# Kernel tuning notes

Hardware: AMD Instinct MI355X
Metric: run time of the kernel (lower is better)

Reference implementation:

```python
import math
import jax, jax.numpy as jnp
import numpy as np

GRAIN = 300   # bilinear / grain dim (gpconv output channels)
PAD = 4       # explicit zero padding before each conv1d / conv2d
POOL = 40     # adaptive pool target (mf_model_pool_dim)

def conv1d_k2(x, w, b):
    # x: [B, L, Cin], w: [Cout, Cin, 2] -> [B, L-1, Cout]
    return (jnp.einsum('blc,oc->blo', x[:, :-1], w[:, :, 0])
            + jnp.einsum('blc,oc->blo', x[:, 1:], w[:, :, 1]) + b)

def kmax_last(x, k):
    # torch-style k-max pooling: top-k values along last axis, original order kept
    idx = jnp.sort(jax.lax.top_k(x, k)[1], axis=-1)
    return jnp.take_along_axis(x, idx, axis=-1)

def kmax_len(x, k):
    # k-max pooling over the length axis (axis=1) of [B, L, C]
    return jnp.swapaxes(kmax_last(jnp.swapaxes(x, 1, 2), k), 1, 2)

def adaptive_max_1d(x, out, axis):
    # torch AdaptiveMaxPool semantics along one axis; windows precomputed statically
    L = x.shape[axis]
    r = np.arange(out)
    starts = (r * L) // out
    ends = -((-(r + 1) * L) // out)
    maxw = int((ends - starts).max())
    off = starts[:, None] + np.arange(maxw)[None, :]
    mask = jnp.asarray(off < ends[:, None])
    idxs = np.minimum(off, L - 1)
    xm = jnp.moveaxis(x, axis, -1)
    g = jnp.where(mask, xm[..., idxs], -jnp.inf)
    return jnp.moveaxis(g.max(-1), -1, axis)

def conv2d_p4(x, w, b):
    y = jax.lax.conv_general_dilated(x, w, (1, 1), [(PAD, PAD), (PAD, PAD)],
                                     dimension_numbers=('NCHW', 'OIHW', 'NCHW'))
    return y + b[None, :, None, None]

def gp_tower(x, w1, b1, w2, b2, w3, b3, k1, k2):
    # multigranular conv tower: zero-pad(4) -> conv1d(k=2) -> tanh -> k-max pool
    g0 = kmax_last(x, GRAIN)                      # [B, L, 300]
    def block(z, w, b, k):
        z = jnp.pad(z, ((0, 0), (PAD, PAD), (0, 0)))
        return kmax_len(jnp.tanh(conv1d_k2(z, w, b)), k)
    p1 = block(x, w1, b1, k1)                     # [B, k1, 300]
    p2 = block(p1, w2, b2, k2)                    # [B, k2, 300]
    p3 = block(p2, w3, b3, 1)                     # [B, 1, 300]
    return jnp.concatenate([g0, p1, p2, p3], axis=1)

def _forward(query, pos_doc, neg_docs, qw1, qb1, qw2, qb2, qw3, qb3,
             dw1, db1, dw2, db2, dw3, db3, bw, bb,
             mw1, mb1, mw2, mb2, mw3, mb3, lw, lb):
    B, Lq, _ = query.shape
    S, _, Ld, _ = neg_docs.shape
    kq1, kq2 = max(4, math.ceil(2 * Lq / 3)), max(4, math.ceil(Lq / 3))
    kd1, kd2 = max(4, math.ceil(2 * Ld / 3)), max(4, math.ceil(Ld / 3))
    qg = gp_tower(query, qw1, qb1, qw2, qb2, qw3, qb3, kq1, kq2)   # [B, Nq, 300]
    docs = jnp.concatenate([pos_doc[None], neg_docs], 0).reshape((S + 1) * B, Ld, -1)
    dg = gp_tower(docs, dw1, db1, dw2, db2, dw3, db3, kd1, kd2)    # [(S+1)B, Nd, 300]
    Nq, Nd = qg.shape[1], dg.shape[1]
    dg = dg.reshape(S + 1, B, Nd, GRAIN)
    # batched bilinear matching + sigmoid (replaces the O(Nq*Nd) per-pair loop)
    qt = jnp.einsum('bqd,de->bqe', qg, bw)
    M = jax.nn.sigmoid(jnp.einsum('bqe,sbje->sbqj', qt, dg) + bb[0])
    M = M.reshape((S + 1) * B, Nq, Nd)
    x = adaptive_max_1d(adaptive_max_1d(M, POOL, 1), POOL, 2)[:, None]  # [N,1,40,40]
    for w, b in ((mw1, mb1), (mw2, mb2), (mw3, mb3)):
        x = jax.nn.sigmoid(conv2d_p4(x, w, b))
        x = adaptive_max_1d(adaptive_max_1d(x, POOL, 2), POOL, 3)
        x = x.max(axis=1, keepdims=True)          # k-max(k=1) over channels
    feat = x[:, 0]                                # [N, 40, 40]
    h = jax.nn.sigmoid(jnp.einsum('nij,j->ni', feat, lw[0]) + lb[0])
    s = jax.nn.sigmoid(h @ lw[0] + lb[0])
    return s.reshape(S + 1, B)                    # row 0 = pos-doc scores

def setup_inputs():
    ks = jax.random.split(jax.random.key(0), 26)
    def n(i, shape, s=0.05):
        return jax.random.normal(ks[i], shape, dtype=jnp.float32) * s
    return dict(
        query=jax.random.normal(ks[0], (16, 239, 1024), dtype=jnp.float32),
        pos_doc=jax.random.normal(ks[1], (16, 479, 1024), dtype=jnp.float32),
        neg_docs=jax.random.normal(ks[2], (4, 16, 479, 1024), dtype=jnp.float32),
        qw1=n(3, (300, 1024, 2)), qb1=n(4, (300,)),
        qw2=n(5, (300, 300, 2)), qb2=n(6, (300,)),
        qw3=n(7, (300, 300, 2)), qb3=n(8, (300,)),
        dw1=n(9, (300, 1024, 2)), db1=n(10, (300,)),
        dw2=n(11, (300, 300, 2)), db2=n(12, (300,)),
        dw3=n(13, (300, 300, 2)), db3=n(14, (300,)),
        bw=n(15, (300, 300)), bb=n(16, (1,)),
        mw1=n(17, (50, 1, 2, 2)), mb1=n(18, (50,)),
        mw2=n(19, (50, 1, 2, 2)), mb2=n(20, (50,)),
        mw3=n(21, (50, 1, 2, 2)), mb3=n(22, (50,)),
        lw=n(23, (1, 40)), lb=n(24, (1,)),
    )

def reference(query, pos_doc, neg_docs, qw1, qb1, qw2, qb2, qw3, qb3,
              dw1, db1, dw2, db2, dw3, db3, bw, bb,
              mw1, mb1, mw2, mb2, mw3, mb3, lw, lb):
    return _forward(query, pos_doc, neg_docs, qw1, qb1, qw2, qb2, qw3, qb3,
                    dw1, db1, dw2, db2, dw3, db3, bw, bb,
                    mw1, mb1, mw2, mb2, mw3, mb3, lw, lb)
```

## Files before the change

kernel.cpp:

```cpp
#include <hip/hip_runtime.h>
#include <hip/hip_bf16.h>
#include <math.h>

typedef unsigned long long ull;
typedef unsigned int uint;
typedef unsigned short ushort_t;

typedef short bf16x8 __attribute__((ext_vector_type(8)));
typedef float floatx4 __attribute__((ext_vector_type(4)));

__device__ inline ushort_t f2b(float f) {
    uint u = __float_as_uint(f);
    u = u + 0x7fffu + ((u >> 16) & 1u);
    return (ushort_t)(u >> 16);
}

__device__ inline uint kmap16(ushort_t u) {
    return (u & 0x8000u) ? (uint)((~u) & 0xFFFFu) : (uint)(u | 0x8000u);
}
__device__ inline ushort_t kinv16(uint k) {
    return (k & 0x8000u) ? (ushort_t)(k ^ 0x8000u) : (ushort_t)((~k) & 0xFFFFu);
}

__device__ inline void async_copy16(const void* g, void* l) {
    __builtin_amdgcn_global_load_lds(
        (const __attribute__((address_space(1))) void*)g,
        (__attribute__((address_space(3))) void*)l, 16, 0, 0);
}

__global__ void prep_w2_kernel(const float* __restrict__ w, ushort_t* __restrict__ Wb,
                               int C, int CP) {
    int CHn = CP / 32;
    int total = CHn * 2 * 20 * 512;
    for (int i = blockIdx.x * blockDim.x + threadIdx.x; i < total;
         i += gridDim.x * blockDim.x) {
        int e = i & 7;
        int lane = (i >> 3) & 63;
        int rest = i >> 9;
        int g = rest % 20;
        int tc = rest / 20;
        int t = tc & 1, c = tc >> 1;
        int o = g * 16 + (lane & 15);
        int ch = c * 32 + (lane >> 4) * 8 + e;
        float v = (o < 300 && ch < C) ? w[((size_t)o * C + ch) * 2 + t] : 0.f;
        Wb[i] = f2b(v);
    }
}

__global__ void prep_bw_kernel(const float* __restrict__ bw, ushort_t* __restrict__ bwb) {
    int i = blockIdx.x * 256 + threadIdx.x;
    if (i >= 320 * 320) return;
    int e = i / 320, d = i - e * 320;
    bwb[i] = (e < 300 && d < 300) ? f2b(bw[d * 300 + e]) : (ushort_t)0;
}

__global__ __launch_bounds__(256) void x_pad_bf16_kernel(
    const float* __restrict__ src, const float* __restrict__ src2, int split_n,
    long long s_nstr, int Lin, ushort_t* __restrict__ dst, int rows)
{
    int r = blockIdx.x, n = blockIdx.y;
    const float* sp = (split_n > 0 && n >= split_n)
                          ? src2 + (size_t)(n - split_n) * s_nstr
                          : src + (size_t)n * s_nstr;
    int g = r - 4;
    ushort_t* dp = dst + ((size_t)n * rows + r) * 1024;
    int c = threadIdx.x * 4;
    ushort4 o = {0, 0, 0, 0};
    if (g >= 0 && g < Lin) {
        float4 v = *(const float4*)&sp[(size_t)g * 1024 + c];
        o.x = f2b(v.x); o.y = f2b(v.y); o.z = f2b(v.z); o.w = f2b(v.w);
    }
    *(ushort4*)&dp[c] = o;
}

template <int CP>
__global__ __launch_bounds__(256, 2) void conv_lds_kernel(
    const ushort_t* __restrict__ xq, long long xq_nstr,
    const ushort_t* __restrict__ xd, long long xd_nstr,
    const ushort_t* __restrict__ Wq, const ushort_t* __restrict__ Wd,
    const float* __restrict__ bq, const float* __restrict__ bd,
    int Lout_q, int Lout_d, int mtiles_q,
    ushort_t* __restrict__ yt)
{
    constexpr int CH = CP / 32;
    constexpr int BUFB = 65 * 64;
    __shared__ ushort_t Abuf[3][65 * 32];

    int mt = blockIdx.x, n = blockIdx.y;
    bool isq = (n < 16);
    if (isq && mt >= mtiles_q) return;
    const ushort_t* x = isq ? xq + (size_t)n * xq_nstr
                            : xd + (size_t)(n - 16) * xd_nstr;
    const ushort_t* W = isq ? Wq : Wd;
    const float* bias = isq ? bq : bd;
    int Lout = isq ? Lout_q : Lout_d;
    int l0 = mt * 64;

    int tid = threadIdx.x, wid = tid >> 6, lane = tid & 63;
    int wn = wid * 80;
    int lrow = lane & 15, quad = lane >> 4;

    int srow = tid >> 2;
    int sslot = (tid & 3) ^ ((tid >> 3) & 3);
    const ushort_t* gMain = x + (size_t)(l0 + srow) * CP + sslot * 8;
    const ushort_t* gXtra = x + (size_t)(l0 + 64) * CP + wid * 8;

    const ushort_t* Bw = W + ((size_t)wid * 5) * 512 + lane * 8;

    int offA[2][4];
#pragma unroll
    for (int t = 0; t < 2; t++)
#pragma unroll
        for (int ms = 0; ms < 4; ms++) {
            int r = ms * 16 + lrow + t;
            offA[t][ms] = r * 64 + ((quad ^ ((r >> 1) & 3)) << 4);
        }

    floatx4 acc[4][5];
#pragma unroll
    for (int i = 0; i < 4; i++)
#pragma unroll
        for (int j = 0; j < 5; j++) acc[i][j] = (floatx4){0.f, 0.f, 0.f, 0.f};

    char* lds0 = (char*)&Abuf[0][0];

    auto STAGE = [&](int cc, int slot) {
        char* lb = lds0 + slot * BUFB;
        async_copy16(gMain + cc * 32, lb + wid * 1024);
        if (lane == 0) async_copy16(gXtra + cc * 32, lb + 4096 + wid * 16);
    };
    auto LOADB = [&](bf16x8 (&bf)[2][5], int cc) {
#pragma unroll
        for (int t = 0; t < 2; t++)
#pragma unroll
            for (int ns = 0; ns < 5; ns++)
                bf[t][ns] = *(const bf16x8*)(Bw + (size_t)((cc * 2 + t) * 20 + ns) * 512);
    };
    auto COMPUTE = [&](bf16x8 (&bf)[2][5], int rslot) {
        const char* ab = lds0 + rslot * BUFB;
        __builtin_amdgcn_s_setprio(1);
#pragma unroll
        for (int t = 0; t < 2; t++) {
            bf16x8 af[4];
#pragma unroll
            for (int ms = 0; ms < 4; ms++)
                af[ms] = *(const bf16x8*)(ab + offA[t][ms]);
#pragma unroll
            for (int ms = 0; ms < 4; ms++)
#pragma unroll
                for (int ns = 0; ns < 5; ns++)
                    acc[ms][ns] = __builtin_amdgcn_mfma_f32_16x16x32_bf16(
                        af[ms], bf[t][ns], acc[ms][ns], 0, 0, 0);
        }
        __builtin_amdgcn_s_setprio(0);
    };
    auto WAITBAR = [&]() {
        asm volatile("s_waitcnt vmcnt(10)" ::: "memory");
        __builtin_amdgcn_s_barrier();
        __builtin_amdgcn_sched_barrier(0);
    };

    bf16x8 bA[2][5], bB[2][5];

    STAGE(0, 0);
    LOADB(bA, 0);
    STAGE(1, 1);

    int sl = 0;
    for (int c = 0; c < CH; c += 2) {
        int rA = sl;
        int rB = rA + 1; if (rB == 3) rB = 0;
        int wA = rB + 1; if (wA == 3) wA = 0;
        int wB = rA;

        WAITBAR();
        LOADB(bB, c + 1);
        __builtin_amdgcn_sched_barrier(0x38F);
        if (c + 2 < CH) STAGE(c + 2, wA);
        COMPUTE(bA, rA);

        WAITBAR();
        if (c + 2 < CH) LOADB(bA, c + 2);
        __builtin_amdgcn_sched_barrier(0x38F);
        if (c + 3 < CH) STAGE(c + 3, wB);
        COMPUTE(bB, rB);

        sl = wA;
    }

    ushort_t* yp = yt + (size_t)n * (320 * 488);
#pragma unroll
    for (int ns = 0; ns < 5; ns++) {
        int o = wn + ns * 16 + lrow;
        if (o >= 300) continue;
        float bo = bias[o];
        ushort_t* orow = yp + (size_t)o * 488;
#pragma unroll
        for (int ms = 0; ms < 4; ms++) {
            int l = l0 + ms * 16 + quad * 4;
            if (l + 3 < Lout) {
                ushort4 v;
                v.x = f2b(tanhf(acc[ms][ns][0] + bo));
                v.y = f2b(tanhf(acc[ms][ns][1] + bo));
                v.z = f2b(tanhf(acc[ms][ns][2] + bo));
                v.w = f2b(tanhf(acc[ms][ns][3] + bo));
                *(ushort4*)&orow[l] = v;
            } else {
#pragma unroll
                for (int r = 0; r < 4; r++)
                    if (l + r < Lout) orow[l + r] = f2b(tanhf(acc[ms][ns][r] + bo));
            }
        }
    }
}

template <int EPT>
__global__ __launch_bounds__(256) void topk16_kernel(
    const ushort_t* __restrict__ src, int CC,
    long long s_n, long long s_c, long long s_e,
    int L, int k,
    ushort_t* __restrict__ out1, long long o1_off, long long o1_n,
    long long o1_c, long long o1_e,
    ushort_t* __restrict__ out2, long long o2_off, long long o2_n,
    long long o2_c, long long o2_e)
{
    __shared__ uint sbuf[257];
    __shared__ uint wtot[4];
    __shared__ uint bsel[2];
    __shared__ uint wsum[4];

    int row = blockIdx.x;
    int n = row / CC, c = row - n * CC;
    const ushort_t* sp = src + (size_t)n * s_n + (size_t)c * s_c;

    int tid = threadIdx.x, lane = tid & 63, wid = tid >> 6;
    int base = tid * EPT;

    uint key[EPT];
    if (EPT == 4 && s_e == 1) {
        ushort4 v = *(const ushort4*)&sp[base];
        key[0] = kmap16(v.x); key[1] = kmap16(v.y);
        key[2] = kmap16(v.z); key[3] = kmap16(v.w);
    } else {
#pragma unroll
        for (int e = 0; e < EPT; e++) {
            int i = base + e;
            key[e] = (i < L) ? kmap16(sp[(size_t)i * s_e]) : 0u;
        }
    }

    uint pmask = 0, pval = 0, rem = (uint)k;
#pragma unroll
    for (int shift = 8; shift >= 0; shift -= 8) {
        sbuf[tid] = 0;
        __syncthreads();
#pragma unroll
        for (int e = 0; e < EPT; e++) {
            int i = base + e;
            if (i < L && (key[e] & pmask) == pval)
                atomicAdd(&sbuf[(key[e] >> shift) & 255], 1u);
        }
        __syncthreads();
        uint sfx = sbuf[tid];
#pragma unroll
        for (int off = 1; off < 64; off <<= 1) {
            uint u2 = __shfl_down(sfx, off);
            if (lane + off < 64) sfx += u2;
        }
        if (lane == 0) wtot[wid] = sfx;
        __syncthreads();
        uint hi = 0;
        for (int w = wid + 1; w < 4; w++) hi += wtot[w];
        sbuf[tid] = sfx + hi;
        if (tid == 0) sbuf[256] = 0;
        __syncthreads();
        uint cg = sbuf[tid], cgn = sbuf[tid + 1];
        if (cg >= rem && cgn < rem) { bsel[0] = (uint)tid; bsel[1] = rem - cgn; }
        __syncthreads();
        pval |= bsel[0] << shift;
        pmask |= 0xFFu << shift;
        rem = bsel[1];
        __syncthreads();
    }

    const uint T = pval;
    uint gtc = 0, eqc = 0;
#pragma unroll
    for (int e = 0; e < EPT; e++) {
        int i = base + e;
        if (i < L) {
            gtc += (key[e] > T) ? 1u : 0u;
            eqc += (key[e] == T) ? 1u : 0u;
        }
    }
    uint pack = (gtc << 16) | eqc;
    uint incl = pack;
#pragma unroll
    for (int off = 1; off < 64; off <<= 1) {
        uint u2 = __shfl_up(incl, off);
        if (lane >= off) incl += u2;
    }
    uint excl = incl - pack;
    if (lane == 63) wsum[wid] = incl;
    __syncthreads();
    uint badd = 0;
    for (int w = 0; w < wid; w++) badd += wsum[w];
    excl += badd;
    uint gt_before = excl >> 16, eq_before = excl & 0xffffu;

    ushort_t* dp1 = out1 + (size_t)o1_off + (size_t)n * o1_n + (size_t)c * o1_c;
    ushort_t* dp2 = out2 ? out2 + (size_t)o2_off + (size_t)n * o2_n + (size_t)c * o2_c
                         : (ushort_t*)0;
#pragma unroll
    for (int e = 0; e < EPT; e++) {
        int i = base + e;
        if (i >= L) break;
        uint kk = key[e];
        if (kk > T) {
            uint pos = gt_before + (eq_before < rem ? eq_before : rem);
            ushort_t v = kinv16(kk);
            dp1[(size_t)pos * o1_e] = v;
            if (dp2) dp2[(size_t)pos * o2_e] = v;
            gt_before++;
        } else if (kk == T) {
            if (eq_before < rem) {
                uint pos = gt_before + eq_before;
                ushort_t v = kinv16(kk);
                dp1[(size_t)pos * o1_e] = v;
                if (dp2) dp2[(size_t)pos * o2_e] = v;
            }
            eq_before++;
        }
    }
}

__global__ __launch_bounds__(256) void topk_cols_kernel(
    const ushort_t* __restrict__ yt2,
    int Lq, int Ld, int kq, int kd,
    ushort_t* __restrict__ qg, int qoff,
    ushort_t* __restrict__ dg, int doff,
    ushort_t* __restrict__ pq, long long pq_nstr,
    ushort_t* __restrict__ pd, long long pd_nstr)
{
    __shared__ __align__(16) ushort_t xin[32][488];
    __shared__ __align__(16) uint hist[32 * 257];
    ushort_t* otile = (ushort_t*)hist;

    int cg = blockIdx.x, n = blockIdx.y;
    int c0 = cg * 32;
    bool isq = (n < 16);
    int L = isq ? Lq : Ld;
    int k = isq ? kq : kd;
    int nd = isq ? n : n - 16;
    int tid = threadIdx.x;

    const ushort_t* src = yt2 + (size_t)n * (320 * 488) + (size_t)c0 * 488;
    for (int i = tid; i < 32 * 61; i += 256) {
        int j = i / 61, s = i - j * 61;
        *(uint4*)&xin[j][s * 8] = *(const uint4*)&src[(size_t)j * 488 + s * 8];
    }
    __syncthreads();

    int g = tid >> 3, r = tid & 7;
    uint* hg = &hist[g * 257];
    bool cval = (c0 + g) < 300;
    int S = (L + 7) >> 3;
    int llo = r * S, lhi = llo + S;
    if (lhi > L) lhi = L;
    if (llo > L) llo = L;

    uint rem = (uint)k;
    uint bsel = 0;
    uint Tt = 0;

#pragma unroll
    for (int round = 0; round < 2; round++) {
        for (int t = r; t < 256; t += 8) hg[t] = 0;
        for (int l = llo; l < lhi; l++) {
            uint key = cval ? kmap16(xin[g][l]) : 0x8000u;
            if (round == 0)
                atomicAdd(&hg[key >> 8], 1u);
            else if ((key >> 8) == bsel)
                atomicAdd(&hg[key & 255u], 1u);
        }
        uint hv[32];
        uint Sr = 0;
        int b0 = r * 32;
#pragma unroll
        for (int t = 0; t < 32; t++) { hv[t] = hg[b0 + t]; Sr += hv[t]; }
        uint suf = Sr;
#pragma unroll
        for (int off = 1; off < 8; off <<= 1) {
            uint u = __shfl_down(suf, off);
            if (r + off < 8) suf += u;
        }
        uint acc = suf - Sr;
        uint found = 0;
#pragma unroll
        for (int t = 31; t >= 0; t--) {
            uint h = hv[t];
            if (!found && acc < rem && acc + h >= rem)
                found = ((uint)(b0 + t) << 16) | (rem - acc);
            acc += h;
        }
#pragma unroll
        for (int off = 1; off < 8; off <<= 1) found |= __shfl_xor(found, off);
        if (round == 0) {
            bsel = found >> 16;
            rem = found & 0xffffu;
        } else {
            Tt = (bsel << 8) | (found >> 16);
            rem = found & 0xffffu;
        }
    }

    uint gtc = 0, eqc = 0;
    for (int l = llo; l < lhi; l++) {
        uint key = cval ? kmap16(xin[g][l]) : 0x8000u;
        gtc += (key > Tt) ? 1u : 0u;
        eqc += (key == Tt) ? 1u : 0u;
    }
    uint pack = (gtc << 16) | eqc, incl = pack;
#pragma unroll
    for (int off = 1; off < 8; off <<= 1) {
        uint u = __shfl_up(incl, off);
        if (r >= off) incl += u;
    }
    uint excl = incl - pack;
    uint gt_b = excl >> 16, eq_b = excl & 0xffffu;

    __syncthreads();

    for (int l = llo; l < lhi; l++) {
        uint key = cval ? kmap16(xin[g][l]) : 0x8000u;
        if (key > Tt) {
            uint pos = gt_b + (eq_b < rem ? eq_b : rem);
            otile[pos * 32 + g] = kinv16(key);
            gt_b++;
        } else if (key == Tt) {
            if (eq_b < rem) otile[(gt_b + eq_b) * 32 + g] = kinv16(key);
            eq_b++;
        }
    }
    __syncthreads();

    ushort_t* d1 = isq ? qg + ((size_t)nd * 480 + qoff) * 320 + c0
                       : dg + ((size_t)nd * 960 + doff) * 320 + c0;
    ushort_t* d2 = 0;
    if (isq) { if (pq) d2 = pq + (size_t)nd * pq_nstr + 4 * 320 + c0; }
    else     { if (pd) d2 = pd + (size_t)nd * pd_nstr + 4 * 320 + c0; }

    for (int i = tid; i < k * 8; i += 256) {
        int p = i >> 3, s = i & 7;
        ushort4 v = *(ushort4*)&otile[p * 32 + s * 4];
        *(ushort4*)&d1[(size_t)p * 320 + s * 4] = v;
        if (d2) *(ushort4*)&d2[(size_t)p * 320 + s * 4] = v;
    }
}

__global__ __launch_bounds__(256) void qt_mfma_kernel(
    const ushort_t* __restrict__ qgb, const ushort_t* __restrict__ bwb,
    ushort_t* __restrict__ qtb)
{
    int mt = blockIdx.x, b = blockIdx.y;
    int tid = threadIdx.x, wid = tid >> 6, lane = tid & 63;
    int wn = wid * 80, lrow = lane & 15, quad = lane >> 4;

    const ushort_t* A = qgb + ((size_t)b * 480 + mt * 48 + lrow) * 320 + quad * 8;
    const ushort_t* B = bwb + (size_t)(wn + lrow) * 320 + quad * 8;

    floatx4 acc[3][5];
#pragma unroll
    for (int i = 0; i < 3; i++)
#pragma unroll
        for (int j = 0; j < 5; j++) acc[i][j] = (floatx4){0.f, 0.f, 0.f, 0.f};

#pragma unroll 5
    for (int c0 = 0; c0 < 320; c0 += 32) {
        bf16x8 af[3], bfr[5];
#pragma unroll
        for (int ms = 0; ms < 3; ms++)
            af[ms] = *(const bf16x8*)&A[(size_t)(ms * 16) * 320 + c0];
#pragma unroll
        for (int ns = 0; ns < 5; ns++)
            bfr[ns] = *(const bf16x8*)&B[(size_t)(ns * 16) * 320 + c0];
#pragma unroll
        for (int ms = 0; ms < 3; ms++)
#pragma unroll
            for (int ns = 0; ns < 5; ns++)
                acc[ms][ns] = __builtin_amdgcn_mfma_f32_16x16x32_bf16(
                    af[ms], bfr[ns], acc[ms][ns], 0, 0, 0);
    }

    ushort_t* out = qtb + ((size_t)b * 480 + mt * 48) * 320;
#pragma unroll
    for (int ms = 0; ms < 3; ms++)
#pragma unroll
        for (int ns = 0; ns < 5; ns++)
#pragma unroll
            for (int r = 0; r < 4; r++)
                out[(size_t)(ms * 16 + quad * 4 + r) * 320 + wn + ns * 16 + lrow] =
                    f2b(acc[ms][ns][r]);
}

__global__ __launch_bounds__(256) void mpool_mfma_kernel(
    const ushort_t* __restrict__ qtb16, const ushort_t* __restrict__ dgb16,
    const float* __restrict__ bb, float* __restrict__ mp)
{
    __shared__ float pool[2 * 12 * 192];

    int jb = blockIdx.x;
    int qb = blockIdx.y;
    int n  = blockIdx.z;
    int b  = n & 15;

    int tid = threadIdx.x;
    int wid = tid >> 6, lane = tid & 63;
    int wm2 = wid >> 1;
    int wm = wm2 * 48, wn = (wid & 1) * 96;
    int lrow = lane & 15, quad = lane >> 4;

    const ushort_t* Abase = qtb16 + ((size_t)b * 480 + qb * 96 + wm) * 320 + quad * 8;
    const ushort_t* Bbase = dgb16 + ((size_t)n * 960 + jb * 192 + wn) * 320 + quad * 8;

    floatx4 acc[3][6];
#pragma unroll
    for (int i = 0; i < 3; i++)
#pragma unroll
        for (int j = 0; j < 6; j++) acc[i][j] = (floatx4){0.f, 0.f, 0.f, 0.f};

#pragma unroll 2
    for (int c0 = 0; c0 < 320; c0 += 32) {
        bf16x8 af[3], bfr[6];
#pragma unroll
        for (int mt = 0; mt < 3; mt++)
            af[mt] = *(const bf16x8*)&Abase[(size_t)(mt * 16 + lrow) * 320 + c0];
#pragma unroll
        for (int nt = 0; nt < 6; nt++)
            bfr[nt] = *(const bf16x8*)&Bbase[(size_t)(nt * 16 + lrow) * 320 + c0];
#pragma unroll
        for (int mt = 0; mt < 3; mt++)
#pragma unroll
            for (int nt = 0; nt < 6; nt++)
                acc[mt][nt] = __builtin_amdgcn_mfma_f32_16x16x32_bf16(
                    af[mt], bfr[nt], acc[mt][nt], 0, 0, 0);
    }

#pragma unroll
    for (int mt = 0; mt < 3; mt++) {
        int g = mt * 4 + quad;
#pragma unroll
        for (int nt = 0; nt < 6; nt++) {
            floatx4 a = acc[mt][nt];
            float rm = fmaxf(fmaxf(a[0], a[1]), fmaxf(a[2], a[3]));
            pool[(wm2 * 12 + g) * 192 + wn + nt * 16 + lrow] = rm;
        }
    }
    __syncthreads();

    if (tid < 64) {
        int qw = tid >> 3, jw = tid & 7;
        int slab = qw >> 2, w = qw & 3;
        float m = -INFINITY;
        const float* pp = &pool[(slab * 12 + w * 3) * 192 + jw * 24];
        for (int g = 0; g < 3; g++)
            for (int cc = 0; cc < 24; cc++)
                m = fmaxf(m, pp[g * 192 + cc]);
        float sig = 1.f / (1.f + expf(-(m + bb[0])));
        mp[(size_t)n * 1600 + (size_t)(qb * 8 + qw) * 40 + (jb * 8 + jw)] = sig;
    }
}

#define OCG 10
__global__ __launch_bounds__(256) void convblock_atomic_kernel(
    const float* __restrict__ X, const float* __restrict__ w,
    const float* __restrict__ bias, uint* __restrict__ Y)
{
    __shared__ float xp[48 * 48];
    __shared__ float ys[47 * 47];
    __shared__ float t1[40 * 47];
    __shared__ float outacc[1600];

    int n = blockIdx.x, t = threadIdx.x;
    int oc0 = blockIdx.y * OCG;
    const float* xn = X + (size_t)n * 1600;
    for (int i = t; i < 48 * 48; i += 256) {
        int r = i / 48, c = i - r * 48;
        int rr = r - 4, cc = c - 4;
        xp[i] = (rr >= 0 && rr < 40 && cc >= 0 && cc < 40) ? xn[rr * 40 + cc] : 0.f;
    }
    for (int i = t; i < 1600; i += 256) outacc[i] = 0.f;
    __syncthreads();

    for (int oc = oc0; oc < oc0 + OCG; oc++) {
        float w00 = w[oc * 4 + 0], w01 = w[oc * 4 + 1];
        float w10 = w[oc * 4 + 2], w11 = w[oc * 4 + 3];
        float bo = bias[oc];
        for (int i = t; i < 47 * 47; i += 256) {
            int r = i / 47, c = i - r * 47;
            float v = xp[r * 48 + c] * w00 + xp[r * 48 + c + 1] * w01
                    + xp[(r + 1) * 48 + c] * w10 + xp[(r + 1) * 48 + c + 1] * w11 + bo;
            ys[i] = 1.f / (1.f + expf(-v));
        }
        __syncthreads();
        for (int i = t; i < 40 * 47; i += 256) {
            int r = i / 47, c = i - r * 47;
            int s = (47 * r) / 40, e = (47 * (r + 1) + 39) / 40;
            float m = ys[s * 47 + c];
            for (int x = s + 1; x < e; x++) m = fmaxf(m, ys[x * 47 + c]);
            t1[i] = m;
        }
        __syncthreads();
        for (int i = t; i < 1600; i += 256) {
            int r = i / 40, c = i - r * 40;
            int s = (47 * c) / 40, e = (47 * (c + 1) + 39) / 40;
            float m = t1[r * 47 + s];
            for (int x = s + 1; x < e; x++) m = fmaxf(m, t1[r * 47 + x]);
            outacc[i] = fmaxf(outacc[i], m);
        }
        __syncthreads();
    }
    for (int i = t; i < 1600; i += 256)
        atomicMax(&Y[(size_t)n * 1600 + i], __float_as_uint(outacc[i]));
}

__global__ __launch_bounds__(64) void head_kernel(
    const float* __restrict__ feat, const float* __restrict__ lw,
    const float* __restrict__ lb, float* __restrict__ out)
{
    __shared__ float hs[40];
    int n = blockIdx.x, t = threadIdx.x;
    const float* f = feat + (size_t)n * 1600;
    if (t < 40) {
        float a = 0.f;
        for (int j = 0; j < 40; j++) a += f[t * 40 + j] * lw[j];
        hs[t] = 1.f / (1.f + expf(-(a + lb[0])));
    }
    __syncthreads();
    if (t == 0) {
        float a = 0.f;
        for (int i = 0; i < 40; i++) a += hs[i] * lw[i];
        out[n] = 1.f / (1.f + expf(-(a + lb[0])));
    }
}

extern "C" void kernel_launch(void* const* d_in, const int* in_sizes, int n_in,
                              void* d_out, int out_size, void* d_ws, size_t ws_size,
                              hipStream_t stream) {
    const float* query    = (const float*)d_in[0];
    const float* pos_doc  = (const float*)d_in[1];
    const float* neg_docs = (const float*)d_in[2];
    const float* qw1 = (const float*)d_in[3];  const float* qb1 = (const float*)d_in[4];
    const float* qw2 = (const float*)d_in[5];  const float* qb2 = (const float*)d_in[6];
    const float* qw3 = (const float*)d_in[7];  const float* qb3 = (const float*)d_in[8];
    const float* dw1 = (const float*)d_in[9];  const float* db1 = (const float*)d_in[10];
    const float* dw2 = (const float*)d_in[11]; const float* db2 = (const float*)d_in[12];
    const float* dw3 = (const float*)d_in[13]; const float* db3 = (const float*)d_in[14];
    const float* bw  = (const float*)d_in[15]; const float* bb  = (const float*)d_in[16];
    const float* mw1 = (const float*)d_in[17]; const float* mb1 = (const float*)d_in[18];
    const float* mw2 = (const float*)d_in[19]; const float* mb2 = (const float*)d_in[20];
    const float* mw3 = (const float*)d_in[21]; const float* mb3 = (const float*)d_in[22];
    const float* lw  = (const float*)d_in[23]; const float* lb  = (const float*)d_in[24];

    float* ws = (float*)d_ws;
    ushort_t* qw1b  = (ushort_t*)(ws + 0);
    ushort_t* qw2b  = (ushort_t*)(ws + 327680);
    ushort_t* qw3b  = (ushort_t*)(ws + 430080);
    ushort_t* dw1b  = (ushort_t*)(ws + 532480);
    ushort_t* dw2b  = (ushort_t*)(ws + 860160);
    ushort_t* dw3b  = (ushort_t*)(ws + 962560);
    ushort_t* bwb   = (ushort_t*)(ws + 1064960);
    ushort_t* qgb16 = (ushort_t*)(ws + 1116160);
    ushort_t* dgb16 = (ushort_t*)(ws + 2344960);
    ushort_t* yt    = (ushort_t*)(ws + 14632960);
    ushort_t* qxb   = (ushort_t*)(ws + 22128640);
    ushort_t* p1q   = (ushort_t*)(ws + 22128640);
    ushort_t* p2q   = (ushort_t*)(ws + 22640640);
    ushort_t* dxb   = (ushort_t*)(ws + 24291328);
    ushort_t* p1d   = (ushort_t*)(ws + 24291328);
    ushort_t* p2d   = (ushort_t*)(ws + 28899328);
    ushort_t* qtb16 = (ushort_t*)(ws + 31459328);
    float*    mp    = ws + 32688128;
    float*    ya    = ws + 32816128;
    float*    yb    = ws + 32944128;
    float*    yc    = ws + 33072128;

    prep_w2_kernel<<<1280, 256, 0, stream>>>(qw1, qw1b, 1024, 1024);
    prep_w2_kernel<<<400, 256, 0, stream>>>(qw2, qw2b, 300, 320);
    prep_w2_kernel<<<400, 256, 0, stream>>>(qw3, qw3b, 300, 320);
    prep_w2_kernel<<<1280, 256, 0, stream>>>(dw1, dw1b, 1024, 1024);
    prep_w2_kernel<<<400, 256, 0, stream>>>(dw2, dw2b, 300, 320);
    prep_w2_kernel<<<400, 256, 0, stream>>>(dw3, dw3b, 300, 320);
    prep_bw_kernel<<<400, 256, 0, stream>>>(bw, bwb);

    {
        dim3 g(264, 16);
        x_pad_bf16_kernel<<<g, 256, 0, stream>>>(query, nullptr, 0,
                                                 239LL * 1024, 239, qxb, 264);
    }
    {
        dim3 g(520, 80);
        x_pad_bf16_kernel<<<g, 256, 0, stream>>>(pos_doc, neg_docs, 16,
                                                 479LL * 1024, 479, dxb, 520);
    }

    topk16_kernel<4><<<16 * 239, 256, 0, stream>>>(
        qxb + 4 * 1024, 239, 264LL * 1024, 1024, 1, 1024, 300,
        qgb16, 0, 480LL * 320, 320, 1,
        nullptr, 0, 0, 0, 0);
    topk16_kernel<4><<<80 * 479, 256, 0, stream>>>(
        dxb + 4 * 1024, 479, 520LL * 1024, 1024, 1, 1024, 300,
        dgb16, 0, 960LL * 320, 320, 1,
        nullptr, 0, 0, 0, 0);

    {
        dim3 g(8, 96);
        conv_lds_kernel<1024><<<g, 256, 0, stream>>>(
            qxb, 264LL * 1024, dxb, 520LL * 1024,
            qw1b, dw1b, qb1, db1, 246, 486, 4, yt);
    }

    hipMemsetAsync(p1q, 0, 16 * 200 * 320 * 2, stream);
    hipMemsetAsync(p2q, 0, 16 * 104 * 320 * 2, stream);
    hipMemsetAsync(p1d, 0, (size_t)80 * 360 * 320 * 2, stream);
    hipMemsetAsync(p2d, 0, (size_t)80 * 200 * 320 * 2, stream);
    hipMemsetAsync(ya, 0, 80 * 1600 * 4, stream);
    hipMemsetAsync(yb, 0, 80 * 1600 * 4, stream);
    hipMemsetAsync(yc, 0, 80 * 1600 * 4, stream);

    {
        dim3 g(10, 96);
        topk_cols_kernel<<<g, 256, 0, stream>>>(
            yt, 246, 486, 160, 320,
            qgb16, 239, dgb16, 479,
            p1q, 200LL * 320, p1d, 360LL * 320);
    }

    {
        dim3 g(6, 96);
        conv_lds_kernel<320><<<g, 256, 0, stream>>>(
            p1q, 200LL * 320, p1d, 360LL * 320,
            qw2b, dw2b, qb2, db2, 167, 327, 3, yt);
    }

    {
        dim3 g(10, 96);
        topk_cols_kernel<<<g, 256, 0, stream>>>(
            yt, 167, 327, 80, 160,
            qgb16, 399, dgb16, 799,
            p2q, 104LL * 320, p2d, 200LL * 320);
    }

    {
        dim3 g(3, 96);
        conv_lds_kernel<320><<<g, 256, 0, stream>>>(
            p2q, 104LL * 320, p2d, 200LL * 320,
            qw3b, dw3b, qb3, db3, 87, 167, 2, yt);
    }

    {
        dim3 g(10, 96);
        topk_cols_kernel<<<g, 256, 0, stream>>>(
            yt, 87, 167, 1, 1,
            qgb16, 479, dgb16, 959,
            nullptr, 0, nullptr, 0);
    }

    {
        dim3 g(10, 16);
        qt_mfma_kernel<<<g, 256, 0, stream>>>(qgb16, bwb, qtb16);
    }
    {
        dim3 g(5, 5, 80);
        mpool_mfma_kernel<<<g, 256, 0, stream>>>(qtb16, dgb16, bb, mp);
    }

    {
        dim3 g(80, 5);
        convblock_atomic_kernel<<<g, 256, 0, stream>>>(mp, mw1, mb1, (uint*)ya);
        convblock_atomic_kernel<<<g, 256, 0, stream>>>(ya, mw2, mb2, (uint*)yb);
        convblock_atomic_kernel<<<g, 256, 0, stream>>>(yb, mw3, mb3, (uint*)yc);
    }
    head_kernel<<<80, 64, 0, stream>>>(yc, lw, lb, (float*)d_out);
}
```

Measured before the change: 1.132 ms.

## Compute g0 top-k with one wavefront per row instead of one block

Replaces the block-per-row radix-select top-k for the g0 grain features with a kernel where each 64-lane wavefront handles one 1024-element row, holding 16 keys per lane and keeping a private LDS histogram per wave. All block-level __syncthreads and cross-wave reductions become wave shuffles, and the key mapping is done two bf16 values at a time with 128-bit loads. The aim is to cut barrier and launch-granularity overhead across roughly 42k rows. Row length, k=300 and unit strides are now hard-coded, and the grid assumes row counts divisible by 4.

```diff
diff --git a/kernel.cpp b/kernel.cpp
--- a/kernel.cpp
+++ b/kernel.cpp
@@ -214,122 +214,108 @@
     }
 }
 
-template <int EPT>
-__global__ __launch_bounds__(256) void topk16_kernel(
-    const ushort_t* __restrict__ src, int CC,
-    long long s_n, long long s_c, long long s_e,
-    int L, int k,
-    ushort_t* __restrict__ out1, long long o1_off, long long o1_n,
-    long long o1_c, long long o1_e,
-    ushort_t* __restrict__ out2, long long o2_off, long long o2_n,
-    long long o2_c, long long o2_e)
+__global__ __launch_bounds__(256) void topk_g0_kernel(
+    const ushort_t* __restrict__ src, int CC, long long s_n,
+    ushort_t* __restrict__ out, long long o_n, long long o_c)
 {
-    __shared__ uint sbuf[257];
-    __shared__ uint wtot[4];
-    __shared__ uint bsel[2];
-    __shared__ uint wsum[4];
-
-    int row = blockIdx.x;
+    __shared__ uint hist[4][257];
+
+    int tid = threadIdx.x, wid = tid >> 6, lane = tid & 63;
+    int row = blockIdx.x * 4 + wid;
     int n = row / CC, c = row - n * CC;
-    const ushort_t* sp = src + (size_t)n * s_n + (size_t)c * s_c;
-
-    int tid = threadIdx.x, lane = tid & 63, wid = tid >> 6;
-    int base = tid * EPT;
-
-    uint key[EPT];
-    if (EPT == 4 && s_e == 1) {
-        ushort4 v = *(const ushort4*)&sp[base];
-        key[0] = kmap16(v.x); key[1] = kmap16(v.y);
-        key[2] = kmap16(v.z); key[3] = kmap16(v.w);
-    } else {
-#pragma unroll
-        for (int e = 0; e < EPT; e++) {
-            int i = base + e;
-            key[e] = (i < L) ? kmap16(sp[(size_t)i * s_e]) : 0u;
-        }
-    }
-
-    uint pmask = 0, pval = 0, rem = (uint)k;
-#pragma unroll
-    for (int shift = 8; shift >= 0; shift -= 8) {
-        sbuf[tid] = 0;
-        __syncthreads();
-#pragma unroll
-        for (int e = 0; e < EPT; e++) {
-            int i = base + e;
-            if (i < L && (key[e] & pmask) == pval)
-                atomicAdd(&sbuf[(key[e] >> shift) & 255], 1u);
-        }
-        __syncthreads();
-        uint sfx = sbuf[tid];
+    const ushort_t* sp = src + (size_t)n * s_n + (size_t)c * 1024;
+
+    const uint* sp32 = (const uint*)(sp + (size_t)lane * 16);
+    uint pk[8];
+    {
+        uint4 va = *(const uint4*)sp32;
+        uint4 vb = *(const uint4*)(sp32 + 4);
+        pk[0] = va.x; pk[1] = va.y; pk[2] = va.z; pk[3] = va.w;
+        pk[4] = vb.x; pk[5] = vb.y; pk[6] = vb.z; pk[7] = vb.w;
+    }
+    uint key[16];
+#pragma unroll
+    for (int i = 0; i < 8; i++) {
+        uint w = pk[i];
+        uint s = w & 0x80008000u;
+        w ^= 0x80008000u | ((s >> 15) * 0x7fffu);
+        key[2 * i] = w & 0xffffu;
+        key[2 * i + 1] = w >> 16;
+    }
+
+    uint* hg = hist[wid];
+    uint rem = 300, bsel = 0, T = 0;
+
+#pragma unroll
+    for (int round = 0; round < 2; round++) {
+#pragma unroll
+        for (int t = 0; t < 4; t++) hg[lane + t * 64] = 0;
+        __builtin_amdgcn_sched_barrier(0);
+        if (round == 0) {
+#pragma unroll
+            for (int e = 0; e < 16; e++) atomicAdd(&hg[key[e] >> 8], 1u);
+        } else {
+#pragma unroll
+            for (int e = 0; e < 16; e++)
+                if ((key[e] >> 8) == bsel) atomicAdd(&hg[key[e] & 255u], 1u);
+        }
+        __builtin_amdgcn_sched_barrier(0);
+        uint hv[4], Sr = 0;
+#pragma unroll
+        for (int t = 0; t < 4; t++) { hv[t] = hg[lane * 4 + t]; Sr += hv[t]; }
+        uint suf = Sr;
 #pragma unroll
         for (int off = 1; off < 64; off <<= 1) {
-            uint u2 = __shfl_down(sfx, off);
-            if (lane + off < 64) sfx += u2;
-        }
-        if (lane == 0) wtot[wid] = sfx;
-        __syncthreads();
-        uint hi = 0;
-        for (int w = wid + 1; w < 4; w++) hi += wtot[w];
-        sbuf[tid] = sfx + hi;
-        if (tid == 0) sbuf[256] = 0;
-        __syncthreads();
-        uint cg = sbuf[tid], cgn = sbuf[tid + 1];
-        if (cg >= rem && cgn < rem) { bsel[0] = (uint)tid; bsel[1] = rem - cgn; }
-        __syncthreads();
-        pval |= bsel[0] << shift;
-        pmask |= 0xFFu << shift;
-        rem = bsel[1];
-        __syncthreads();
-    }
-
-    const uint T = pval;
+            uint u = __shfl_down(suf, off);
+            if (lane + off < 64) suf += u;
+        }
+        uint acc = suf - Sr;
+        uint found = 0;
+#pragma unroll
+        for (int t = 3; t >= 0; t--) {
+            uint h = hv[t];
+            if (!found && acc < rem && acc + h >= rem)
+                found = ((uint)(lane * 4 + t) << 16) | (rem - acc);
+            acc += h;
+        }
+#pragma unroll
+        for (int off = 1; off < 64; off <<= 1) found |= __shfl_xor(found, off);
+        if (round == 0) {
+            bsel = found >> 16;
+            rem = found & 0xffffu;
+        } else {
+            T = (bsel << 8) | (found >> 16);
+            rem = found & 0xffffu;
+        }
+        __builtin_amdgcn_sched_barrier(0);
+    }
+
     uint gtc = 0, eqc = 0;
 #pragma unroll
-    for (int e = 0; e < EPT; e++) {
-        int i = base + e;
-        if (i < L) {
-            gtc += (key[e] > T) ? 1u : 0u;
-            eqc += (key[e] == T) ? 1u : 0u;
-        }
-    }
-    uint pack = (gtc << 16) | eqc;
-    uint incl = pack;
+    for (int e = 0; e < 16; e++) {
+        gtc += (key[e] > T) ? 1u : 0u;
+        eqc += (key[e] == T) ? 1u : 0u;
+    }
+    uint pack = (gtc << 16) | eqc, incl = pack;
 #pragma unroll
     for (int off = 1; off < 64; off <<= 1) {
-        uint u2 = __shfl_up(incl, off);
-        if (lane >= off) incl += u2;
+        uint u = __shfl_up(incl, off);
+        if (lane >= off) incl += u;
     }
     uint excl = incl - pack;
-    if (lane == 63) wsum[wid] = incl;
-    __syncthreads();
-    uint badd = 0;
-    for (int w = 0; w < wid; w++) badd += wsum[w];
-    excl += badd;
-    uint gt_before = excl >> 16, eq_before = excl & 0xffffu;
-
-    ushort_t* dp1 = out1 + (size_t)o1_off + (size_t)n * o1_n + (size_t)c * o1_c;
-    ushort_t* dp2 = out2 ? out2 + (size_t)o2_off + (size_t)n * o2_n + (size_t)c * o2_c
-                         : (ushort_t*)0;
-#pragma unroll
-    for (int e = 0; e < EPT; e++) {
-        int i = base + e;
-        if (i >= L) break;
+    uint gt_b = excl >> 16, eq_b = excl & 0xffffu;
+
+    ushort_t* dp = out + (size_t)n * o_n + (size_t)c * o_c;
+#pragma unroll
+    for (int e = 0; e < 16; e++) {
         uint kk = key[e];
         if (kk > T) {
-            uint pos = gt_before + (eq_before < rem ? eq_before : rem);
-            ushort_t v = kinv16(kk);
-            dp1[(size_t)pos * o1_e] = v;
-            if (dp2) dp2[(size_t)pos * o2_e] = v;
-            gt_before++;
+            uint pos = gt_b + (eq_b < rem ? eq_b : rem);
+            dp[pos] = kinv16(kk);
+            gt_b++;
         } else if (kk == T) {
-            if (eq_before < rem) {
-                uint pos = gt_before + eq_before;
-                ushort_t v = kinv16(kk);
-                dp1[(size_t)pos * o1_e] = v;
-                if (dp2) dp2[(size_t)pos * o2_e] = v;
-            }
-            eq_before++;
+            if (eq_b < rem) dp[gt_b + eq_b] = kinv16(kk);
+            eq_b++;
         }
     }
 }
@@ -704,14 +690,10 @@
                                                  479LL * 1024, 479, dxb, 520);
     }
 
-    topk16_kernel<4><<<16 * 239, 256, 0, stream>>>(
-        qxb + 4 * 1024, 239, 264LL * 1024, 1024, 1, 1024, 300,
-        qgb16, 0, 480LL * 320, 320, 1,
-        nullptr, 0, 0, 0, 0);
-    topk16_kernel<4><<<80 * 479, 256, 0, stream>>>(
-        dxb + 4 * 1024, 479, 520LL * 1024, 1024, 1, 1024, 300,
-        dgb16, 0, 960LL * 320, 320, 1,
-        nullptr, 0, 0, 0, 0);
+    topk_g0_kernel<<<(16 * 239) / 4, 256, 0, stream>>>(
+        qxb + 4 * 1024, 239, 264LL * 1024, qgb16, 480LL * 320, 320);
+    topk_g0_kernel<<<(80 * 479) / 4, 256, 0, stream>>>(
+        dxb + 4 * 1024, 479, 520LL * 1024, dgb16, 960LL * 320, 320);
 
     {
         dim3 g(8, 96);
```

Result: faster. 1.101 ms (-2.8%).
